# Kernel optimization log

Hardware: AMD Instinct MI355X
Metric: run time of the kernel (lower is better)

Reference implementation:

```python
import jax, jax.numpy as jnp
import numpy as np
import math

T, B, E, H = 1024, 4, 512, 8
HD = E // H

def setup_inputs() -> dict:
    key = jax.random.key(0)
    ks = jax.random.split(key, 6)
    return {
        "query": jax.random.normal(ks[0], (T, B, E), dtype=jnp.float32),
        "dist": jax.random.normal(ks[1], (B, T, T, H), dtype=jnp.float32) * 0.1,
        "in_proj_weight": jax.random.normal(ks[2], (3 * E, E), dtype=jnp.float32) * 0.02,
        "in_proj_bias": jax.random.normal(ks[3], (3 * E,), dtype=jnp.float32) * 0.02,
        "out_proj_weight": jax.random.normal(ks[4], (E, E), dtype=jnp.float32) * 0.02,
        "out_proj_bias": jax.random.normal(ks[5], (E,), dtype=jnp.float32) * 0.02,
    }

def reference(query, dist, in_proj_weight, in_proj_bias, out_proj_weight, out_proj_bias):
    t, b, e = query.shape
    # packed in-projection (self-attention: q=k=v=query)
    qkv = query @ in_proj_weight.T + in_proj_bias          # [T,B,3E]
    q, k, v = jnp.split(qkv, 3, axis=-1)                   # each [T,B,E]
    def heads(x):
        return x.reshape(t, b * H, HD).transpose(1, 0, 2)  # [B*H,T,HD]
    q, k, v = heads(q), heads(k), heads(v)
    q = q / math.sqrt(HD)
    attn = jnp.einsum('bte,bse->bts', q, k)                # [B*H,T,T]
    # distance/structure bias: [B,T,T,H] -> [B,H,T,T] -> [B*H,T,T]
    bias = jnp.transpose(dist, (0, 3, 1, 2)).reshape(b * H, t, t)
    attn = jax.nn.softmax(attn + bias, axis=-1)
    out = jnp.einsum('bts,bse->bte', attn, v)              # [B*H,T,HD]
    out = out.transpose(1, 0, 2).reshape(t, b, e)          # [T,B,E]
    out = out @ out_proj_weight.T + out_proj_bias
    return out
```

## Files before the change

kernel.cpp:

```cpp
#include <hip/hip_runtime.h>
#include <math.h>

typedef __bf16 bf16;
typedef bf16 bf16x8 __attribute__((ext_vector_type(8)));
typedef bf16 bf16x4 __attribute__((ext_vector_type(4)));
typedef float f32x4 __attribute__((ext_vector_type(4)));

#define T_DIM 1024
#define B_DIM 4
#define E_DIM 512
#define H_DIM 8
#define HD_DIM 64
#define BH_DIM 32
#define SPLIT 4
#define S_PER (T_DIM / SPLIT)

__device__ __forceinline__ f32x4 mfma16(bf16x8 a, bf16x8 b, f32x4 c) {
    return __builtin_amdgcn_mfma_f32_16x16x32_bf16(a, b, c, 0, 0, 0);
}

__device__ __forceinline__ bf16x4 cvt4(f32x4 v) {
    bf16x4 o;
    o[0] = (bf16)v[0]; o[1] = (bf16)v[1]; o[2] = (bf16)v[2]; o[3] = (bf16)v[3];
    return o;
}

#define CVT_Q_V   524288
#define CVT_W1_V  196608
__global__ __launch_bounds__(256)
void cvt_all(const float* __restrict__ q, const float* __restrict__ w1,
             const float* __restrict__ w2, bf16* __restrict__ qo,
             bf16* __restrict__ w1o, bf16* __restrict__ w2o) {
    long v = (long)blockIdx.x * 256 + threadIdx.x;
    const float* src; bf16* dst;
    if (v < CVT_Q_V)                { src = q;  dst = qo; }
    else if (v < CVT_Q_V + CVT_W1_V){ v -= CVT_Q_V;  src = w1; dst = w1o; }
    else                            { v -= CVT_Q_V + CVT_W1_V; src = w2; dst = w2o; }
    f32x4 f = *(const f32x4*)(src + v * 4);
    *(bf16x4*)(dst + v * 4) = cvt4(f);
}

__global__ __launch_bounds__(256)
void bias_transpose(const float* __restrict__ dist, bf16* __restrict__ bias_t) {
    __shared__ __align__(16) bf16 tile[8 * 1032];
    const int bt = blockIdx.x;
    const int b = bt >> 10, t = bt & 1023;
    const int tid = threadIdx.x;
    const float* src = dist + ((long)bt << 13) + tid * 32;
    const int s0 = tid * 4;
    float v[32];
#pragma unroll
    for (int j = 0; j < 8; j++) {
        f32x4 f = *(const f32x4*)(src + j * 4);
        v[j * 4 + 0] = f[0]; v[j * 4 + 1] = f[1];
        v[j * 4 + 2] = f[2]; v[j * 4 + 3] = f[3];
    }
#pragma unroll
    for (int h = 0; h < 8; h++)
#pragma unroll
        for (int si = 0; si < 4; si++)
            tile[h * 1032 + s0 + si] = (bf16)v[si * 8 + h];
    __syncthreads();
#pragma unroll
    for (int rep = 0; rep < 4; rep++) {
        int slot = rep * 256 + tid;
        int h = slot >> 7;
        int sc = (slot & 127) * 8;
        bf16x8 o = *(const bf16x8*)&tile[h * 1032 + sc];
        *(bf16x8*)&bias_t[((long)(b * 8 + h) * T_DIM + t) * T_DIM + sc] = o;
    }
}

template<int TM, int TN, int MODE>
__global__ __launch_bounds__(256)
void gemm_t(const bf16* __restrict__ A, const bf16* __restrict__ Bt,
            const float* __restrict__ bias, int K, int N,
            float* __restrict__ out, bf16* __restrict__ qb,
            bf16* __restrict__ kb, bf16* __restrict__ vb) {
    constexpr int FM = TM / 32, FN = TN / 32;
    constexpr int PA = TM / 64, PB = TN / 64;
    __shared__ __align__(16) bf16 As[TM * 72];
    __shared__ __align__(16) bf16 Bs[TN * 72];
    const int tid  = threadIdx.x;
    const int lane = tid & 63;
    const int wave = tid >> 6;
    const int quad = lane >> 4;
    const int l15  = lane & 15;
    const int wm = wave & 1, wn = wave >> 1;
    const int m0 = blockIdx.x * TM, n0 = blockIdx.y * TN;

    f32x4 acc[FM][FN] = {};

    const int sr = tid >> 2;
    const int sc = (tid & 3) * 16;

    bf16x8 ra[PA][2], rb[PB][2];
#pragma unroll
    for (int p = 0; p < PA; p++) {
        const bf16* src = &A[(long)(m0 + p * 64 + sr) * K + sc];
        ra[p][0] = *(const bf16x8*)(src);
        ra[p][1] = *(const bf16x8*)(src + 8);
    }
#pragma unroll
    for (int p = 0; p < PB; p++) {
        const bf16* src = &Bt[(long)(n0 + p * 64 + sr) * K + sc];
        rb[p][0] = *(const bf16x8*)(src);
        rb[p][1] = *(const bf16x8*)(src + 8);
    }

    for (int k0 = 0; k0 < K; k0 += 64) {
        __syncthreads();
#pragma unroll
        for (int p = 0; p < PA; p++) {
            *(bf16x8*)&As[(p * 64 + sr) * 72 + sc]     = ra[p][0];
            *(bf16x8*)&As[(p * 64 + sr) * 72 + sc + 8] = ra[p][1];
        }
#pragma unroll
        for (int p = 0; p < PB; p++) {
            *(bf16x8*)&Bs[(p * 64 + sr) * 72 + sc]     = rb[p][0];
            *(bf16x8*)&Bs[(p * 64 + sr) * 72 + sc + 8] = rb[p][1];
        }
        __syncthreads();

        if (k0 + 64 < K) {
            const int kn = k0 + 64;
#pragma unroll
            for (int p = 0; p < PA; p++) {
                const bf16* src = &A[(long)(m0 + p * 64 + sr) * K + kn + sc];
                ra[p][0] = *(const bf16x8*)(src);
                ra[p][1] = *(const bf16x8*)(src + 8);
            }
#pragma unroll
            for (int p = 0; p < PB; p++) {
                const bf16* src = &Bt[(long)(n0 + p * 64 + sr) * K + kn + sc];
                rb[p][0] = *(const bf16x8*)(src);
                rb[p][1] = *(const bf16x8*)(src + 8);
            }
        }

#pragma unroll
        for (int kk = 0; kk < 64; kk += 32) {
            bf16x8 af[FM], bfr[FN];
#pragma unroll
            for (int mb = 0; mb < FM; mb++)
                af[mb] = *(const bf16x8*)&As[(wm * (TM / 2) + mb * 16 + l15) * 72 + kk + quad * 8];
#pragma unroll
            for (int nb = 0; nb < FN; nb++)
                bfr[nb] = *(const bf16x8*)&Bs[(wn * (TN / 2) + nb * 16 + l15) * 72 + kk + quad * 8];
#pragma unroll
            for (int mb = 0; mb < FM; mb++)
#pragma unroll
                for (int nb = 0; nb < FN; nb++)
                    acc[mb][nb] = mfma16(af[mb], bfr[nb], acc[mb][nb]);
        }
    }

#pragma unroll
    for (int mb = 0; mb < FM; mb++) {
#pragma unroll
        for (int nb = 0; nb < FN; nb++) {
            int n = n0 + wn * (TN / 2) + nb * 16 + l15;
            float bv = bias[n];
#pragma unroll
            for (int r = 0; r < 4; r++) {
                int m = m0 + wm * (TM / 2) + mb * 16 + quad * 4 + r;
                float v = acc[mb][nb][r] + bv;
                if (MODE == 0) {
                    out[(long)m * N + n] = v;
                } else {
                    int t = m >> 2, b = m & 3;
                    int sec = n >> 9, j = n & 511;
                    int h = j >> 6, hd = j & 63;
                    int bh = b * 8 + h;
                    if (sec == 0)
                        qb[((long)bh * T_DIM + t) * HD_DIM + hd] = (bf16)(v * 0.125f);
                    else if (sec == 1)
                        kb[((long)bh * T_DIM + t) * HD_DIM + hd] = (bf16)v;
                    else
                        vb[((long)bh * HD_DIM + hd) * T_DIM + t] = (bf16)v;
                }
            }
        }
    }
}

__global__ __launch_bounds__(256)
void attn_kernel(const bf16* __restrict__ qb, const bf16* __restrict__ kb,
                 const bf16* __restrict__ vb, const bf16* __restrict__ bias_t,
                 float* __restrict__ po, float* __restrict__ pl) {
    __shared__ __align__(16) bf16 Ks[64 * 72];
    __shared__ __align__(16) bf16 Vts[64 * 72];
    __shared__ __align__(16) bf16 Ps[4 * 16 * 72];
    const int tid  = threadIdx.x;
    const int lane = tid & 63;
    const int wave = tid >> 6;
    const int quad = lane >> 4;
    const int l15  = lane & 15;
    const int bid  = blockIdx.x;
    const int bh   = (bid >> 4) & 31;
    const int qt   = bid & 15;
    const int split = bid >> 9;
    const int s0   = split * S_PER;
    const int b    = bh >> 3;
    const int qrow = qt * 64 + wave * 16 + l15;

    bf16x8 qa0 = *(const bf16x8*)&qb[((long)bh * T_DIM + qrow) * HD_DIM + quad * 8];
    bf16x8 qa1 = *(const bf16x8*)&qb[((long)bh * T_DIM + qrow) * HD_DIM + 32 + quad * 8];

    f32x4 oacc[4] = {};
    float lsum[4] = {0.f, 0.f, 0.f, 0.f};

    const int r0 = tid >> 3;
    const int c0 = (tid & 7) * 8;

    const bf16* dp = bias_t + ((long)bh * T_DIM + qt * 64 + wave * 16 + quad * 4) * T_DIM;

    bf16x8 pk0, pk1, pv0, pv1;
    float pbias[16];
    pk0 = *(const bf16x8*)&kb[((long)bh * T_DIM + s0 + r0) * HD_DIM + c0];
    pk1 = *(const bf16x8*)&kb[((long)bh * T_DIM + s0 + r0 + 32) * HD_DIM + c0];
    pv0 = *(const bf16x8*)&vb[((long)bh * HD_DIM + r0) * T_DIM + s0 + c0];
    pv1 = *(const bf16x8*)&vb[((long)bh * HD_DIM + r0 + 32) * T_DIM + s0 + c0];
#pragma unroll
    for (int r = 0; r < 4; r++)
#pragma unroll
        for (int nb = 0; nb < 4; nb++)
            pbias[r * 4 + nb] = (float)dp[(long)r * T_DIM + s0 + nb * 16 + l15];

    for (int st = s0; st < s0 + S_PER; st += 64) {
        __syncthreads();
        *(bf16x8*)&Ks[r0 * 72 + c0]         = pk0;
        *(bf16x8*)&Ks[(r0 + 32) * 72 + c0]  = pk1;
        *(bf16x8*)&Vts[r0 * 72 + c0]        = pv0;
        *(bf16x8*)&Vts[(r0 + 32) * 72 + c0] = pv1;
        __syncthreads();

        if (st + 64 < s0 + S_PER) {
            const int sn = st + 64;
            pk0 = *(const bf16x8*)&kb[((long)bh * T_DIM + sn + r0) * HD_DIM + c0];
            pk1 = *(const bf16x8*)&kb[((long)bh * T_DIM + sn + r0 + 32) * HD_DIM + c0];
            pv0 = *(const bf16x8*)&vb[((long)bh * HD_DIM + r0) * T_DIM + sn + c0];
            pv1 = *(const bf16x8*)&vb[((long)bh * HD_DIM + r0 + 32) * T_DIM + sn + c0];
        }

        f32x4 sacc[4] = {};
        __builtin_amdgcn_s_setprio(1);
#pragma unroll
        for (int kk = 0; kk < 64; kk += 32) {
            bf16x8 a = (kk == 0) ? qa0 : qa1;
#pragma unroll
            for (int nb = 0; nb < 4; nb++) {
                bf16x8 bfr = *(const bf16x8*)&Ks[(nb * 16 + l15) * 72 + kk + quad * 8];
                sacc[nb] = mfma16(a, bfr, sacc[nb]);
            }
        }
        __builtin_amdgcn_s_setprio(0);

        bf16* pw = &Ps[wave * 16 * 72];
#pragma unroll
        for (int r = 0; r < 4; r++) {
            float rs = 0.f;
#pragma unroll
            for (int nb = 0; nb < 4; nb++) {
                float p = __expf(sacc[nb][r] + pbias[r * 4 + nb]);
                rs += p;
                pw[(quad * 4 + r) * 72 + nb * 16 + l15] = (bf16)p;
            }
            lsum[r] += rs;
        }

        if (st + 64 < s0 + S_PER) {
            const int sn = st + 64;
#pragma unroll
            for (int r = 0; r < 4; r++)
#pragma unroll
                for (int nb = 0; nb < 4; nb++)
                    pbias[r * 4 + nb] = (float)dp[(long)r * T_DIM + sn + nb * 16 + l15];
        }

        __builtin_amdgcn_s_setprio(1);
#pragma unroll
        for (int kk = 0; kk < 64; kk += 32) {
            bf16x8 ap = *(const bf16x8*)&pw[l15 * 72 + kk + quad * 8];
#pragma unroll
            for (int nb = 0; nb < 4; nb++) {
                bf16x8 bv2 = *(const bf16x8*)&Vts[(nb * 16 + l15) * 72 + kk + quad * 8];
                oacc[nb] = mfma16(ap, bv2, oacc[nb]);
            }
        }
        __builtin_amdgcn_s_setprio(0);
    }

#pragma unroll
    for (int r = 0; r < 4; r++) {
#pragma unroll
        for (int msk = 1; msk < 16; msk <<= 1)
            lsum[r] += __shfl_xor(lsum[r], msk);
    }

    float* pob = po + (long)split * (BH_DIM * T_DIM * HD_DIM);
#pragma unroll
    for (int nb = 0; nb < 4; nb++) {
#pragma unroll
        for (int r = 0; r < 4; r++) {
            int t  = qt * 64 + wave * 16 + quad * 4 + r;
            int hd = nb * 16 + l15;
            pob[((long)bh * T_DIM + t) * HD_DIM + hd] = oacc[nb][r];
        }
    }
    if (l15 == 0) {
#pragma unroll
        for (int r = 0; r < 4; r++) {
            int t = qt * 64 + wave * 16 + quad * 4 + r;
            pl[(long)split * (BH_DIM * T_DIM) + bh * T_DIM + t] = lsum[r];
        }
    }
}

__global__ __launch_bounds__(256)
void combine(const float* __restrict__ po, const float* __restrict__ pl,
             bf16* __restrict__ ctxb) {
    const int gid = blockIdx.x * 256 + threadIdx.x;
    const int hd4 = gid & 15;
    const int t   = (gid >> 4) & 1023;
    const int bh  = gid >> 14;
    const long base = ((long)bh * T_DIM + t) * HD_DIM + hd4 * 4;
    f32x4 o = {};
    float l = 0.f;
#pragma unroll
    for (int s = 0; s < SPLIT; s++) {
        o += *(const f32x4*)&po[(long)s * (BH_DIM * T_DIM * HD_DIM) + base];
        l += pl[(long)s * (BH_DIM * T_DIM) + bh * T_DIM + t];
    }
    float inv = 1.f / l;
    f32x4 r = o * inv;
    const int b = bh >> 3, hh = bh & 7;
    *(bf16x4*)&ctxb[((long)t * B_DIM + b) * E_DIM + hh * HD_DIM + hd4 * 4] = cvt4(r);
}

extern "C" void kernel_launch(void* const* d_in, const int* in_sizes, int n_in,
                              void* d_out, int out_size, void* d_ws, size_t ws_size,
                              hipStream_t stream) {
    const float* query = (const float*)d_in[0];
    const float* dist  = (const float*)d_in[1];
    const float* win   = (const float*)d_in[2];
    const float* bin   = (const float*)d_in[3];
    const float* wout  = (const float*)d_in[4];
    const float* bout  = (const float*)d_in[5];
    float* out = (float*)d_out;

    bf16* bias_t = (bf16*)d_ws;
    bf16* qb   = bias_t + ((long)BH_DIM * T_DIM * T_DIM);
    bf16* kb   = qb + (1 << 21);
    bf16* vb   = kb + (1 << 21);
    bf16* qbf  = vb + (1 << 21);
    bf16* w1bf = qbf + (1 << 21);
    bf16* w2bf = w1bf + 786432;
    bf16* ctxb = w2bf + 262144;
    float* po  = (float*)(ctxb + (1 << 21));
    float* pl  = po + (long)SPLIT * BH_DIM * T_DIM * HD_DIM;

    cvt_all<<<dim3(3072), 256, 0, stream>>>(query, win, wout, qbf, w1bf, w2bf);
    bias_transpose<<<dim3(B_DIM * T_DIM), 256, 0, stream>>>(dist, bias_t);
    gemm_t<128, 128, 1><<<dim3(32, 12), 256, 0, stream>>>(
        qbf, w1bf, bin, 512, 1536, nullptr, qb, kb, vb);
    attn_kernel<<<dim3(512 * SPLIT), 256, 0, stream>>>(qb, kb, vb, bias_t, po, pl);
    combine<<<dim3(2048), 256, 0, stream>>>(po, pl, ctxb);
    gemm_t<128, 64, 0><<<dim3(32, 8), 256, 0, stream>>>(
        ctxb, w2bf, bout, 512, 512, out, nullptr, nullptr, nullptr);
}
```

Before: 287.1 us.

## Fuse prep kernels, double-buffer GEMM shared memory, and retile GEMMs

The conversion and bias-transpose kernels are merged into one launch, which saves a kernel launch and lets the two jobs overlap. The GEMM now double-buffers its shared-memory tiles, cutting the per-iteration syncs from two to one. Both GEMMs get smaller M tiles (64x192 and 64x64), giving more blocks to fill the CUs. The cost is more LDS per block and possibly less reuse per tile.

```diff
diff --git a/kernel.cpp b/kernel.cpp
--- a/kernel.cpp
+++ b/kernel.cpp
@@ -28,21 +28,21 @@
 #define CVT_Q_V   524288
 #define CVT_W1_V  196608
 __global__ __launch_bounds__(256)
-void cvt_all(const float* __restrict__ q, const float* __restrict__ w1,
-             const float* __restrict__ w2, bf16* __restrict__ qo,
-             bf16* __restrict__ w1o, bf16* __restrict__ w2o) {
-    long v = (long)blockIdx.x * 256 + threadIdx.x;
-    const float* src; bf16* dst;
-    if (v < CVT_Q_V)                { src = q;  dst = qo; }
-    else if (v < CVT_Q_V + CVT_W1_V){ v -= CVT_Q_V;  src = w1; dst = w1o; }
-    else                            { v -= CVT_Q_V + CVT_W1_V; src = w2; dst = w2o; }
-    f32x4 f = *(const f32x4*)(src + v * 4);
-    *(bf16x4*)(dst + v * 4) = cvt4(f);
-}
-
-__global__ __launch_bounds__(256)
-void bias_transpose(const float* __restrict__ dist, bf16* __restrict__ bias_t) {
+void prep(const float* __restrict__ dist, bf16* __restrict__ bias_t,
+          const float* __restrict__ q, const float* __restrict__ w1,
+          const float* __restrict__ w2, bf16* __restrict__ qo,
+          bf16* __restrict__ w1o, bf16* __restrict__ w2o) {
     __shared__ __align__(16) bf16 tile[8 * 1032];
+    if (blockIdx.x >= 4096) {
+        long v = (long)(blockIdx.x - 4096) * 256 + threadIdx.x;
+        const float* src; bf16* dst;
+        if (v < CVT_Q_V)                { src = q;  dst = qo; }
+        else if (v < CVT_Q_V + CVT_W1_V){ v -= CVT_Q_V;  src = w1; dst = w1o; }
+        else                            { v -= CVT_Q_V + CVT_W1_V; src = w2; dst = w2o; }
+        f32x4 f = *(const f32x4*)(src + v * 4);
+        *(bf16x4*)(dst + v * 4) = cvt4(f);
+        return;
+    }
     const int bt = blockIdx.x;
     const int b = bt >> 10, t = bt & 1023;
     const int tid = threadIdx.x;
@@ -79,8 +79,8 @@
             bf16* __restrict__ kb, bf16* __restrict__ vb) {
     constexpr int FM = TM / 32, FN = TN / 32;
     constexpr int PA = TM / 64, PB = TN / 64;
-    __shared__ __align__(16) bf16 As[TM * 72];
-    __shared__ __align__(16) bf16 Bs[TN * 72];
+    __shared__ __align__(16) bf16 As[2][TM * 72];
+    __shared__ __align__(16) bf16 Bs[2][TN * 72];
     const int tid  = threadIdx.x;
     const int lane = tid & 63;
     const int wave = tid >> 6;
@@ -108,22 +108,25 @@
         rb[p][1] = *(const bf16x8*)(src + 8);
     }
 
-    for (int k0 = 0; k0 < K; k0 += 64) {
+    const int NK = K >> 6;
+    for (int i = 0; i < NK; i++) {
+        const int cur = i & 1;
+        bf16* as = As[cur];
+        bf16* bs = Bs[cur];
+#pragma unroll
+        for (int p = 0; p < PA; p++) {
+            *(bf16x8*)&as[(p * 64 + sr) * 72 + sc]     = ra[p][0];
+            *(bf16x8*)&as[(p * 64 + sr) * 72 + sc + 8] = ra[p][1];
+        }
+#pragma unroll
+        for (int p = 0; p < PB; p++) {
+            *(bf16x8*)&bs[(p * 64 + sr) * 72 + sc]     = rb[p][0];
+            *(bf16x8*)&bs[(p * 64 + sr) * 72 + sc + 8] = rb[p][1];
+        }
         __syncthreads();
-#pragma unroll
-        for (int p = 0; p < PA; p++) {
-            *(bf16x8*)&As[(p * 64 + sr) * 72 + sc]     = ra[p][0];
-            *(bf16x8*)&As[(p * 64 + sr) * 72 + sc + 8] = ra[p][1];
-        }
-#pragma unroll
-        for (int p = 0; p < PB; p++) {
-            *(bf16x8*)&Bs[(p * 64 + sr) * 72 + sc]     = rb[p][0];
-            *(bf16x8*)&Bs[(p * 64 + sr) * 72 + sc + 8] = rb[p][1];
-        }
-        __syncthreads();
-
-        if (k0 + 64 < K) {
-            const int kn = k0 + 64;
+
+        if (i + 1 < NK) {
+            const int kn = (i + 1) << 6;
 #pragma unroll
             for (int p = 0; p < PA; p++) {
                 const bf16* src = &A[(long)(m0 + p * 64 + sr) * K + kn + sc];
@@ -143,10 +146,10 @@
             bf16x8 af[FM], bfr[FN];
 #pragma unroll
             for (int mb = 0; mb < FM; mb++)
-                af[mb] = *(const bf16x8*)&As[(wm * (TM / 2) + mb * 16 + l15) * 72 + kk + quad * 8];
+                af[mb] = *(const bf16x8*)&as[(wm * (TM / 2) + mb * 16 + l15) * 72 + kk + quad * 8];
 #pragma unroll
             for (int nb = 0; nb < FN; nb++)
-                bfr[nb] = *(const bf16x8*)&Bs[(wn * (TN / 2) + nb * 16 + l15) * 72 + kk + quad * 8];
+                bfr[nb] = *(const bf16x8*)&bs[(wn * (TN / 2) + nb * 16 + l15) * 72 + kk + quad * 8];
 #pragma unroll
             for (int mb = 0; mb < FM; mb++)
 #pragma unroll
@@ -201,7 +204,6 @@
     const int qt   = bid & 15;
     const int split = bid >> 9;
     const int s0   = split * S_PER;
-    const int b    = bh >> 3;
     const int qrow = qt * 64 + wave * 16 + l15;
 
     bf16x8 qa0 = *(const bf16x8*)&qb[((long)bh * T_DIM + qrow) * HD_DIM + quad * 8];
@@ -360,12 +362,12 @@
     float* po  = (float*)(ctxb + (1 << 21));
     float* pl  = po + (long)SPLIT * BH_DIM * T_DIM * HD_DIM;
 
-    cvt_all<<<dim3(3072), 256, 0, stream>>>(query, win, wout, qbf, w1bf, w2bf);
-    bias_transpose<<<dim3(B_DIM * T_DIM), 256, 0, stream>>>(dist, bias_t);
-    gemm_t<128, 128, 1><<<dim3(32, 12), 256, 0, stream>>>(
+    prep<<<dim3(7168), 256, 0, stream>>>(dist, bias_t, query, win, wout,
+                                         qbf, w1bf, w2bf);
+    gemm_t<64, 192, 1><<<dim3(64, 8), 256, 0, stream>>>(
         qbf, w1bf, bin, 512, 1536, nullptr, qb, kb, vb);
     attn_kernel<<<dim3(512 * SPLIT), 256, 0, stream>>>(qb, kb, vb, bias_t, po, pl);
     combine<<<dim3(2048), 256, 0, stream>>>(po, pl, ctxb);
-    gemm_t<128, 64, 0><<<dim3(32, 8), 256, 0, stream>>>(
+    gemm_t<64, 64, 0><<<dim3(64, 8), 256, 0, stream>>>(
         ctxb, w2bf, bout, 512, 512, out, nullptr, nullptr, nullptr);
 }
```

Result: faster. 277.7 us (-3.3%).
